# Optimization experiments

Hardware: AMD Instinct MI355X
Metric: run time of the kernel (lower is better)

## Reference

```python
import jax, jax.numpy as jnp
import numpy as np

QLEN, BSZ, HID, NH, HD = 512, 8, 1024, 16, 64
PLEN = 2 * QLEN
SCALE = 1.0 / (HD ** 0.5)
BIG_NUM = 1e30
EPS = 1e-5


def _rel_shift(x, klen):
    # x: [b, n, i, j] -> shifted [b, n, i, klen], same raw-reshape trick as torch.
    b, n, i, j = x.shape
    x = x.reshape(b, n, j, i)[:, :, 1:, :]
    x = x.reshape(b, n, i, j - 1)
    return x[:, :, :, :klen]


def setup_inputs() -> dict:
    key = jax.random.key(0)
    ks = jax.random.split(key, 12)
    s = jnp.float32(0.02)
    return {
        "hidden_states": jax.random.normal(ks[0], (QLEN, BSZ, HID), jnp.float32),
        "position_embed": jax.random.normal(ks[1], (PLEN, BSZ, HID), jnp.float32),
        "segment_embed": jax.random.uniform(ks[2], (QLEN, QLEN, BSZ, 2), jnp.float32),
        "attn_mask": jnp.zeros((QLEN, QLEN, BSZ, 1), jnp.float32),
        "q": jax.random.normal(ks[3], (HID, NH, HD), jnp.float32) * s,
        "k": jax.random.normal(ks[4], (HID, NH, HD), jnp.float32) * s,
        "v": jax.random.normal(ks[5], (HID, NH, HD), jnp.float32) * s,
        "r": jax.random.normal(ks[6], (HID, NH, HD), jnp.float32) * s,
        "o": jax.random.normal(ks[7], (HID, NH, HD), jnp.float32) * s,
        "r_w_bias": jax.random.normal(ks[8], (NH, HD), jnp.float32) * s,
        "r_r_bias": jax.random.normal(ks[9], (NH, HD), jnp.float32) * s,
        "r_s_bias": jax.random.normal(ks[10], (NH, HD), jnp.float32) * s,
        "seg_mat": jax.random.normal(ks[11], (2, NH, HD), jnp.float32) * s,
        "ln_gamma": jnp.ones((HID,), jnp.float32),
        "ln_beta": jnp.zeros((HID,), jnp.float32),
    }


def reference(hidden_states, position_embed, segment_embed, attn_mask,
              q, k, v, r, o, r_w_bias, r_r_bias, r_s_bias, seg_mat,
              ln_gamma, ln_beta):
    query = jnp.einsum('ibh,hnd->ibnd', hidden_states, q)
    key_ = jnp.einsum('ibh,hnd->ibnd', hidden_states, k)
    value = jnp.einsum('ibh,hnd->ibnd', hidden_states, v)
    key_r = jnp.einsum('ibh,hnd->ibnd', position_embed, r)

    # content score
    ac = jnp.einsum('ibnd,jbnd->bnij', query + r_w_bias, key_)
    # relative position score with rel_shift
    bd = jnp.einsum('ibnd,jbnd->bnij', query + r_r_bias, key_r)
    bd = _rel_shift(bd, ac.shape[3])
    # segment score
    ef = jnp.einsum('ibnd,snd->ibns', query + r_s_bias, seg_mat)
    ef = jnp.einsum('ijbs,ibns->bnij', segment_embed, ef)

    attn_score = (ac + bd + ef) * SCALE
    attn_score = attn_score - BIG_NUM * jnp.transpose(attn_mask, (2, 3, 0, 1))
    attn_prob = jax.nn.softmax(attn_score, axis=-1)  # dropout is identity in eval

    attn_out = jnp.einsum('bnij,jbnd->ibnd', attn_prob, value)
    attn_out = jnp.einsum('ibnd,hnd->ibh', attn_out, o)

    x = attn_out + hidden_states
    mu = jnp.mean(x, axis=-1, keepdims=True)
    var = jnp.mean((x - mu) ** 2, axis=-1, keepdims=True)
    return (x - mu) * jax.lax.rsqrt(var + EPS) * ln_gamma + ln_beta
```

## Files before the change

### kernel.cpp

```cpp
#include <hip/hip_runtime.h>
#include <hip/hip_bf16.h>

#define I_LEN 512
#define BSZ   8
#define HIDN  1024
#define NHEAD 16
#define HDIM  64
#define PLEN_ 1024
#define SCALE_F 0.125f
#define BIGNUM 1e30f
#define LN_EPS 1e-5f

typedef unsigned int   u32;
typedef unsigned short u16;
typedef __attribute__((ext_vector_type(8))) short bf16x8;
typedef __attribute__((ext_vector_type(4))) float f32x4;

__device__ __forceinline__ float bflo(u32 w) { return __uint_as_float(w << 16); }
__device__ __forceinline__ float bfhi(u32 w) { return __uint_as_float(w & 0xffff0000u); }
__device__ __forceinline__ u16 f2bf(float x) {
  u32 u = __float_as_uint(x);
  return (u16)((u + 0x7fffu + ((u >> 16) & 1u)) >> 16);
}
__device__ __forceinline__ void bf8_to_f(const uint4 v, float* f) {
  f[0] = bflo(v.x); f[1] = bfhi(v.x);
  f[2] = bflo(v.y); f[3] = bfhi(v.y);
  f[4] = bflo(v.z); f[5] = bfhi(v.z);
  f[6] = bflo(v.w); f[7] = bfhi(v.w);
}

#define GLOAD_LDS16(gp, lp) __builtin_amdgcn_global_load_lds( \
    (const __attribute__((address_space(1))) void*)(gp),      \
    (__attribute__((address_space(3))) void*)(lp), 16, 0, 0)

__global__ __launch_bounds__(256)
void proj_gemm(const u16* __restrict__ Hb, const float* __restrict__ pos,
               const u16* __restrict__ Wqt, const u16* __restrict__ Wkt,
               const u16* __restrict__ Wvt, const u16* __restrict__ Wrt,
               u16* __restrict__ Qh, u16* __restrict__ Kf,
               u16* __restrict__ Vh, u16* __restrict__ Krf) {
  constexpr int K = 1024;
  __shared__ union {
    struct { u16 As[2 * 8192]; u16 Bs[2 * 8192]; } st;
    u16 epi[4][64 * 68];
    u16 epiK[128 * 137];
  } sm;
  u16* As = sm.st.As;
  u16* Bs = sm.st.Bs;
  const int id = blockIdx.x;
  const int low = id & 7;
  const int rest = id >> 3;
  const int bx = rest & 7;
  const int grp = low + 8 * (rest >> 3);
  const int by = grp & 31;
  const int z = grp >> 5;
  const u16* Bt; u16* C;
  if (z == 0)      { Bt = Wqt; C = Qh;  }
  else if (z == 1) { Bt = Wkt; C = Kf;  }
  else if (z == 2) { Bt = Wvt; C = Vh;  }
  else if (z == 3) { Bt = Wrt; C = Krf; }
  else             { Bt = Wrt; C = Krf; }
  const float* Apos = pos + (size_t)((z == 4) ? 4096 : 0) * 1024;
  const int bm = by * 128, bn = bx * 128;
  const int tid = threadIdx.x, wv = tid >> 6, lane = tid & 63;
  const int l15 = lane & 15, g = lane >> 4;
  const int wr = wv >> 1, wc = wv & 1;

#define STAGE_B_P(BUF, K0)                                                    \
  _Pragma("unroll")                                                           \
  for (int p = 0; p < 4; ++p) {                                               \
    const int unit = (wv * 4 + p) * 64 + lane;                                \
    const int row = unit >> 3, up = unit & 7, cc = up ^ (row & 7);            \
    GLOAD_LDS16(&Bt[(size_t)(bn + row) * K + (K0) + cc * 8],                  \
                &Bs[(BUF) * 8192 + unit * 8]);                                \
  }
#define STAGE_A16_P(BUF, K0)                                                  \
  _Pragma("unroll")                                                           \
  for (int p = 0; p < 4; ++p) {                                               \
    const int unit = (wv * 4 + p) * 64 + lane;                                \
    const int row = unit >> 3, up = unit & 7, cc = up ^ (row & 7);            \
    GLOAD_LDS16(&Hb[(size_t)(bm + row) * K + (K0) + cc * 8],                  \
                &As[(BUF) * 8192 + unit * 8]);                                \
  }
#define STAGE_A32_P(BUF, K0)                                                  \
  _Pragma("unroll")                                                           \
  for (int p = 0; p < 4; ++p) {                                               \
    const int unit = p * 256 + tid;                                           \
    const int row = unit >> 3, up = unit & 7, cc = up ^ (row & 7);            \
    const float* src = &Apos[(size_t)(bm + row) * K + (K0) + cc * 8];         \
    const float4 f0 = *(const float4*)src;                                    \
    const float4 f1 = *(const float4*)(src + 4);                              \
    ushort4 h0, h1;                                                           \
    h0.x = f2bf(f0.x); h0.y = f2bf(f0.y); h0.z = f2bf(f0.z); h0.w = f2bf(f0.w); \
    h1.x = f2bf(f1.x); h1.y = f2bf(f1.y); h1.z = f2bf(f1.z); h1.w = f2bf(f1.w); \
    *(ushort4*)&As[(BUF) * 8192 + unit * 8] = h0;                             \
    *(ushort4*)&As[(BUF) * 8192 + unit * 8 + 4] = h1;                         \
  }
#define COMPUTE_TILE(CUR)                                                     \
  {                                                                           \
    const u16* Ac = &As[(CUR) * 8192];                                        \
    const u16* Bc = &Bs[(CUR) * 8192];                                        \
    _Pragma("unroll")                                                         \
    for (int h = 0; h < 2; ++h) {                                             \
      bf16x8 af[4], bfv[4];                                                   \
      _Pragma("unroll")                                                       \
      for (int m = 0; m < 4; ++m) {                                           \
        const int row = wr * 64 + m * 16 + l15;                               \
        af[m] = *(const bf16x8*)&Ac[row * 64 + ((h * 4 + g) ^ (row & 7)) * 8];\
      }                                                                       \
      _Pragma("unroll")                                                       \
      for (int n = 0; n < 4; ++n) {                                           \
        const int col = wc * 64 + n * 16 + l15;                               \
        bfv[n] = *(const bf16x8*)&Bc[col * 64 + ((h * 4 + g) ^ (col & 7)) * 8];\
      }                                                                       \
      _Pragma("unroll")                                                       \
      for (int m = 0; m < 4; ++m)                                             \
        _Pragma("unroll")                                                     \
        for (int n = 0; n < 4; ++n)                                           \
          acc[m][n] = __builtin_amdgcn_mfma_f32_16x16x32_bf16(af[m], bfv[n],  \
                                                              acc[m][n], 0, 0, 0); \
    }                                                                         \
  }

  f32x4 acc[4][4];
#pragma unroll
  for (int m = 0; m < 4; ++m)
#pragma unroll
    for (int n = 0; n < 4; ++n) acc[m][n] = (f32x4){0.f, 0.f, 0.f, 0.f};

  if (z < 3) {
    STAGE_B_P(0, 0);
    STAGE_A16_P(0, 0);
    int cur = 0;
    for (int t = 0; t < 16; ++t) {
      if (t < 15) {
        const int k1 = (t + 1) * 64;
        STAGE_B_P(cur ^ 1, k1);
        STAGE_A16_P(cur ^ 1, k1);
        asm volatile("s_waitcnt vmcnt(8)" ::: "memory");
      } else {
        asm volatile("s_waitcnt vmcnt(0)" ::: "memory");
      }
      __builtin_amdgcn_s_barrier();
      __builtin_amdgcn_sched_barrier(0);
      COMPUTE_TILE(cur);
      __builtin_amdgcn_s_barrier();
      cur ^= 1;
    }
  } else {
    STAGE_B_P(0, 0);
    STAGE_A32_P(0, 0);
    __syncthreads();
    int cur = 0;
    for (int t = 0; t < 16; ++t) {
      if (t < 15) {
        const int k1 = (t + 1) * 64;
        STAGE_B_P(cur ^ 1, k1);
        STAGE_A32_P(cur ^ 1, k1);
      }
      COMPUTE_TILE(cur);
      __syncthreads();
      cur ^= 1;
    }
  }

  if (z == 1 || z >= 3) {
    u16* E128 = sm.epiK;
#pragma unroll
    for (int m = 0; m < 4; ++m)
#pragma unroll
      for (int nf = 0; nf < 4; ++nf)
#pragma unroll
        for (int r = 0; r < 4; ++r)
          E128[(wr * 64 + m * 16 + g * 4 + r) * 137 + wc * 64 + nf * 16 + l15] =
              f2bf(acc[m][nf][r]);
    __syncthreads();
    const int tK = (z == 1) ? by : (by + ((z == 4) ? 32 : 0));
    const int TS = (z == 1) ? 32 : 64;
#pragma unroll
    for (int q = 0; q < 8; ++q) {
      const int rid = wv * 8 + q;
      const int n_loc = rid >> 4, b_ = (rid >> 1) & 7, h = rid & 1;
      union { u16 us[8]; uint4 qv; } o;
#pragma unroll
      for (int e = 0; e < 8; ++e)
        o.us[e] = E128[(l15 * 8 + b_) * 137 + n_loc * 64 + h * 32 + g * 8 + e];
      const int head = bx * 2 + n_loc;
      const size_t base = (((size_t)(b_ * 16 + head) * TS + tK) * 2 + h) * 512 + lane * 8;
      *(uint4*)&C[base] = o.qv;
    }
  } else {
    u16* slice = sm.epi[wv];
    __syncthreads();
#pragma unroll
    for (int m = 0; m < 4; ++m)
#pragma unroll
      for (int nf = 0; nf < 4; ++nf)
#pragma unroll
        for (int r = 0; r < 4; ++r)
          slice[(m * 16 + g * 4 + r) * 68 + nf * 16 + l15] = f2bf(acc[m][nf][r]);
#pragma unroll
    for (int it = 0; it < 8; ++it) {
      const int rl = it * 8 + (lane >> 3);
      const int cl = (lane & 7) * 8;
      const ushort4 a = *(const ushort4*)&slice[rl * 68 + cl];
      const ushort4 b2 = *(const ushort4*)&slice[rl * 68 + cl + 4];
      const int row = bm + wr * 64 + rl;
      const int col = bn + wc * 64 + cl;
      const size_t idx = ((size_t)((row & 7) * 16 + (col >> 6)) * 512 + (row >> 3)) * 64 + (col & 63);
      *(ushort4*)&C[idx] = a;
      *(ushort4*)&C[idx + 4] = b2;
    }
  }
}

__global__ __launch_bounds__(256)
void vrepack_kernel(u16* __restrict__ V) {
  __shared__ u16 tile[64][72];
  const int bn = blockIdx.x, slab = blockIdx.y;
  const int t = threadIdx.x;
  const size_t base = ((size_t)bn * 8 + slab) * 4096;
  {
    const int jl = t >> 2, c0 = (t & 3) * 16;
    const uint4 v0 = *(const uint4*)&V[base + jl * 64 + c0];
    const uint4 v1 = *(const uint4*)&V[base + jl * 64 + c0 + 8];
    *(uint4*)&tile[jl][c0] = v0;
    *(uint4*)&tile[jl][c0 + 8] = v1;
  }
  __syncthreads();
  const int lane = t & 63, g = lane >> 4, l15 = lane & 15;
#pragma unroll
  for (int w = 0; w < 2; ++w) {
    const int run = w * 4 + (t >> 6);
    const int c = run >> 1, h = run & 1;
    union { u16 us[8]; uint4 qv; } o;
#pragma unroll
    for (int e = 0; e < 8; ++e) o.us[e] = tile[h * 32 + g * 8 + e][16 * c + l15];
    *(uint4*)&V[base + run * 512 + lane * 8] = o.qv;
  }
}

__global__ __launch_bounds__(256)
void hcvt_kernel(const float* __restrict__ hidden, const float* __restrict__ ow,
                 u16* __restrict__ Hb, u16* __restrict__ Wob) {
  const size_t i = (size_t)blockIdx.x * 256 + threadIdx.x;
  const float* src; u16* dst; size_t off;
  if (i < 524288) { src = hidden; dst = Hb; off = i * 8; }
  else            { src = ow;     dst = Wob; off = (i - 524288) * 8; }
  const float4 a = *(const float4*)&src[off];
  const float4 b = *(const float4*)&src[off + 4];
  ushort4 o0, o1;
  o0.x = f2bf(a.x); o0.y = f2bf(a.y); o0.z = f2bf(a.z); o0.w = f2bf(a.w);
  o1.x = f2bf(b.x); o1.y = f2bf(b.y); o1.z = f2bf(b.z); o1.w = f2bf(b.w);
  *(ushort4*)&dst[off] = o0;
  *(ushort4*)&dst[off + 4] = o1;
}

__global__ __launch_bounds__(256)
void wtrans_kernel(const float* __restrict__ W0, const float* __restrict__ W1,
                   const float* __restrict__ W2, const float* __restrict__ W3,
                   u16* __restrict__ T0, u16* __restrict__ T1,
                   u16* __restrict__ T2, u16* __restrict__ T3) {
  __shared__ u16 tile[64][72];
  const int z = blockIdx.z;
  const float* W = (z == 0) ? W0 : ((z == 1) ? W1 : ((z == 2) ? W2 : W3));
  u16* T = (z == 0) ? T0 : ((z == 1) ? T1 : ((z == 2) ? T2 : T3));
  const int h0 = blockIdx.y * 64, nd0 = blockIdx.x * 64;
  const int t = threadIdx.x;
  {
    const int hr = t >> 2, c0 = (t & 3) * 16;
#pragma unroll
    for (int q = 0; q < 4; ++q) {
      const float4 f = *(const float4*)&W[(size_t)(h0 + hr) * 1024 + nd0 + c0 + q * 4];
      tile[hr][c0 + q * 4 + 0] = f2bf(f.x);
      tile[hr][c0 + q * 4 + 1] = f2bf(f.y);
      tile[hr][c0 + q * 4 + 2] = f2bf(f.z);
      tile[hr][c0 + q * 4 + 3] = f2bf(f.w);
    }
  }
  __syncthreads();
  const int ndr = t >> 2, hc0 = (t & 3) * 16;
  union { u16 us[16]; uint4 qv[2]; } o;
#pragma unroll
  for (int e = 0; e < 16; ++e) o.us[e] = tile[hc0 + e][ndr];
  uint4* dst = (uint4*)&T[(size_t)(nd0 + ndr) * 1024 + h0 + hc0];
  dst[0] = o.qv[0]; dst[1] = o.qv[1];
}

__global__ __launch_bounds__(256)
void setrans_kernel(const float* __restrict__ sege, const float* __restrict__ amask,
                    u16* __restrict__ SE4, u16* __restrict__ MK) {
  const int i = blockIdx.x;
  const int j = blockIdx.y * 256 + threadIdx.x;
  const float* sp = &sege[((size_t)i * 512 + j) * 16];
  const float* mp = &amask[((size_t)i * 512 + j) * 8];
  float se[16], mk[8];
#pragma unroll
  for (int q = 0; q < 4; ++q) {
    const float4 f = *(const float4*)(sp + q * 4);
    se[q * 4 + 0] = f.x; se[q * 4 + 1] = f.y; se[q * 4 + 2] = f.z; se[q * 4 + 3] = f.w;
  }
#pragma unroll
  for (int q = 0; q < 2; ++q) {
    const float4 f = *(const float4*)(mp + q * 4);
    mk[q * 4 + 0] = f.x; mk[q * 4 + 1] = f.y; mk[q * 4 + 2] = f.z; mk[q * 4 + 3] = f.w;
  }
#pragma unroll
  for (int b = 0; b < 8; ++b) {
    const u32 pk = (u32)f2bf(se[b * 2]) | ((u32)f2bf(se[b * 2 + 1]) << 16);
    const size_t plane = ((size_t)b * 512 + i) * 512 + j;
    *(u32*)&SE4[plane * 2] = pk;
    MK[plane] = f2bf(BIGNUM * mk[b]);
  }
}

__global__ __launch_bounds__(256)
void seg_e_kernel(const u16* __restrict__ Qh, const float* __restrict__ rsb,
                  const float* __restrict__ segm, float* __restrict__ E) {
  const int gt = blockIdx.x * 256 + threadIdx.x;
  const int i = gt >> 7, bb = (gt >> 4) & 7, n = gt & 15;
  const size_t base = (((size_t)bb * 16 + n) * 512 + i) * 64;
  float e0 = 0.f, e1 = 0.f;
#pragma unroll
  for (int u8 = 0; u8 < 8; ++u8) {
    const uint4 qv = *(const uint4*)&Qh[base + u8 * 8];
    float qf[8];
    bf8_to_f(qv, qf);
#pragma unroll
    for (int w = 0; w < 8; ++w) {
      const int d = u8 * 8 + w;
      const float q = qf[w] + rsb[n * HDIM + d];
      e0 += q * segm[n * HDIM + d];
      e1 += q * segm[HIDN + n * HDIM + d];
    }
  }
  E[(size_t)gt * 2 + 0] = e0;
  E[(size_t)gt * 2 + 1] = e1;
}

__global__ __launch_bounds__(256)
void attn_mfma(const u16* __restrict__ Qh, const u16* __restrict__ Kf,
               const u16* __restrict__ Vf, const u16* __restrict__ Krf,
               const float* __restrict__ E, const u16* __restrict__ SE4,
               const u16* __restrict__ MK, const float* __restrict__ rwb,
               const float* __restrict__ rrb, u16* __restrict__ AOb) {
  __shared__ u16 Pl[4][16 * 64];
  const int id = blockIdx.x;
  const int b = id & 7, n = (id >> 3) & 15;
  const int i0 = (id >> 7) * 64;
  const int bn = b * 16 + n;
  const int t = threadIdx.x, wv = t >> 6, lane = t & 63;
  const int l15 = lane & 15, g = lane >> 4;
  const int irow0 = i0 + wv * 16;
  u16* Pw = Pl[wv];
  const int bn64 = bn * 64;

  bf16x8 qcf[2], qrf[2];
#pragma unroll
  for (int h = 0; h < 2; ++h) {
    const int d0 = 32 * h + g * 8;
    const uint4 qv = *(const uint4*)&Qh[((size_t)bn * 512 + irow0 + l15) * 64 + d0];
    float qf[8]; bf8_to_f(qv, qf);
    union { u16 us[8]; bf16x8 v; } ua, ub;
#pragma unroll
    for (int w = 0; w < 8; ++w) {
      ua.us[w] = f2bf((qf[w] + rwb[n * HDIM + d0 + w]) * SCALE_F);
      ub.us[w] = f2bf((qf[w] + rrb[n * HDIM + d0 + w]) * SCALE_F);
    }
    qcf[h] = ua.v; qrf[h] = ub.v;
  }

  float e0v[4], e1v[4], lrun[4];
  f32x4 accO[4];
#pragma unroll
  for (int r = 0; r < 4; ++r) {
    const int i = irow0 + 4 * g + r;
    const float2 ee = *(const float2*)&E[((size_t)(i * BSZ + b) * NHEAD + n) * 2];
    e0v[r] = ee.x * SCALE_F; e1v[r] = ee.y * SCALE_F;
    lrun[r] = 0.f;
  }
#pragma unroll
  for (int c = 0; c < 4; ++c) accO[c] = (f32x4){0.f, 0.f, 0.f, 0.f};

  for (int jb = 0; jb < I_LEN; jb += 64) {
    u32 sev[4][4]; u16 mkv[4][4];
#pragma unroll
    for (int c = 0; c < 4; ++c)
#pragma unroll
      for (int r = 0; r < 4; ++r) {
        const size_t plane = ((size_t)b * 512 + (irow0 + 4 * g + r)) * 512 + jb + 16 * c + l15;
        sev[c][r] = *(const u32*)&SE4[plane * 2];
        mkv[c][r] = MK[plane];
      }
    bf16x8 vf[4][2];
#pragma unroll
    for (int c = 0; c < 4; ++c) {
      const u16* vp = &Vf[((((size_t)bn * 8 + (jb >> 6)) * 4 + c) * 2) * 512 + lane * 8];
      vf[c][0] = *(const bf16x8*)vp;
      vf[c][1] = *(const bf16x8*)(vp + 512);
    }
    f32x4 S[4];
#pragma unroll
    for (int c = 0; c < 4; ++c) S[c] = (f32x4){0.f, 0.f, 0.f, 0.f};
#pragma unroll
    for (int c = 0; c < 4; ++c) {
      const u16* kp = &Kf[(((size_t)bn * 32 + (jb >> 4) + c) * 2) * 512 + lane * 8];
      S[c] = __builtin_amdgcn_mfma_f32_16x16x32_bf16(qcf[0], *(const bf16x8*)kp, S[c], 0, 0, 0);
      S[c] = __builtin_amdgcn_mfma_f32_16x16x32_bf16(qcf[1], *(const bf16x8*)(kp + 512), S[c], 0, 0, 0);
    }
    const int tb = (jb + 496 - irow0) >> 4;
    f32x4 T[5];
#pragma unroll
    for (int c = 0; c < 5; ++c) T[c] = (f32x4){0.f, 0.f, 0.f, 0.f};
#pragma unroll
    for (int c = 0; c < 5; ++c) {
      const u16* kp = &Krf[(((size_t)bn * 64 + tb + c) * 2) * 512 + lane * 8];
      T[c] = __builtin_amdgcn_mfma_f32_16x16x32_bf16(qrf[0], *(const bf16x8*)kp, T[c], 0, 0, 0);
      T[c] = __builtin_amdgcn_mfma_f32_16x16x32_bf16(qrf[1], *(const bf16x8*)(kp + 512), T[c], 0, 0, 0);
    }
    float bd[4][4];
#pragma unroll
    for (int r = 0; r < 4; ++r) {
      const int ii = 4 * g + r;
      const int pos = (lane & 48) | ((l15 - ii) & 15);
      float bp[5];
#pragma unroll
      for (int c = 0; c < 5; ++c) bp[c] = __shfl(T[c][r], pos, 64);
      const bool sel = l15 >= ii;
#pragma unroll
      for (int c = 0; c < 4; ++c) bd[c][r] = sel ? bp[c + 1] : bp[c];
    }
#pragma unroll
    for (int c = 0; c < 4; ++c)
#pragma unroll
      for (int r = 0; r < 4; ++r) {
        const u32 sev_ = sev[c][r];
        const float s = S[c][r] + bd[c][r] + bflo(sev_) * e0v[r] + bfhi(sev_) * e1v[r]
                        - bflo((u32)mkv[c][r]);
        const float p = __expf(s);
        S[c][r] = p;
        lrun[r] += p;
      }
#pragma unroll
    for (int c = 0; c < 4; ++c)
#pragma unroll
      for (int r = 0; r < 4; ++r) {
        const int ii = 4 * g + r;
        Pw[ii * 64 + ((16 * c + l15) ^ ((ii & 7) << 3))] = f2bf(S[c][r]);
      }
    const bf16x8 pa0 = *(const bf16x8*)&Pw[l15 * 64 + ((g * 8) ^ ((l15 & 7) << 3))];
    const bf16x8 pa1 = *(const bf16x8*)&Pw[l15 * 64 + ((32 + g * 8) ^ ((l15 & 7) << 3))];
#pragma unroll
    for (int c = 0; c < 4; ++c) {
      accO[c] = __builtin_amdgcn_mfma_f32_16x16x32_bf16(pa0, vf[c][0], accO[c], 0, 0, 0);
      accO[c] = __builtin_amdgcn_mfma_f32_16x16x32_bf16(pa1, vf[c][1], accO[c], 0, 0, 0);
    }
  }
#pragma unroll
  for (int r = 0; r < 4; ++r) {
#pragma unroll
    for (int o = 1; o < 16; o <<= 1) lrun[r] += __shfl_xor(lrun[r], o);
  }
#pragma unroll
  for (int c = 0; c < 4; ++c)
#pragma unroll
    for (int r = 0; r < 4; ++r) {
      const int ii = 4 * g + r;
      AOb[(size_t)(irow0 + ii) * 8192 + bn64 + 16 * c + l15] = f2bf(accO[c][r] / lrun[r]);
    }
}

__global__ __launch_bounds__(256)
void oproj_gemm(const u16* __restrict__ A, const u16* __restrict__ Wob,
                const float* __restrict__ Res, float* __restrict__ C) {
  constexpr int K = 1024;
  __shared__ u16 As[2 * 4096];
  __shared__ u16 Bs[2 * 8192];
  const int id = blockIdx.x;
  const int low = id & 7;
  const int rest = id >> 3;
  const int bx = rest & 7;
  const int by = low + 8 * (rest >> 3);
  const int bm = by * 64, bn = bx * 128;
  const int tid = threadIdx.x, wv = tid >> 6, lane = tid & 63;
  const int l15 = lane & 15, g = lane >> 4;
  const int wr = wv >> 1, wc = wv & 1;

#define STAGE_O(BUF, K0)                                                      \
  _Pragma("unroll")                                                           \
  for (int p = 0; p < 2; ++p) {                                               \
    const int unit = (wv * 2 + p) * 64 + lane;                                \
    const int row = unit >> 3, up = unit & 7, cc = up ^ (row & 7);            \
    GLOAD_LDS16(&A[(size_t)(bm + row) * K + (K0) + cc * 8],                   \
                &As[(BUF) * 4096 + unit * 8]);                                \
  }                                                                           \
  _Pragma("unroll")                                                           \
  for (int p = 0; p < 4; ++p) {                                               \
    const int unit = (wv * 4 + p) * 64 + lane;                                \
    const int row = unit >> 3, up = unit & 7, cc = up ^ (row & 7);            \
    GLOAD_LDS16(&Wob[(size_t)(bn + row) * K + (K0) + cc * 8],                 \
                &Bs[(BUF) * 8192 + unit * 8]);                                \
  }

  f32x4 acc[2][4];
#pragma unroll
  for (int m = 0; m < 2; ++m)
#pragma unroll
    for (int n = 0; n < 4; ++n) acc[m][n] = (f32x4){0.f, 0.f, 0.f, 0.f};

  STAGE_O(0, 0);
  int cur = 0;
  for (int t = 0; t < 16; ++t) {
    if (t < 15) {
      STAGE_O(cur ^ 1, (t + 1) * 64);
      asm volatile("s_waitcnt vmcnt(6)" ::: "memory");
    } else {
      asm volatile("s_waitcnt vmcnt(0)" ::: "memory");
    }
    __builtin_amdgcn_s_barrier();
    __builtin_amdgcn_sched_barrier(0);
    const u16* Ac = &As[cur * 4096];
    const u16* Bc = &Bs[cur * 8192];
#pragma unroll
    for (int h = 0; h < 2; ++h) {
      bf16x8 af[2], bfv[4];
#pragma unroll
      for (int m = 0; m < 2; ++m) {
        const int row = wr * 32 + m * 16 + l15;
        af[m] = *(const bf16x8*)&Ac[row * 64 + ((h * 4 + g) ^ (row & 7)) * 8];
      }
#pragma unroll
      for (int n = 0; n < 4; ++n) {
        const int col = wc * 64 + n * 16 + l15;
        bfv[n] = *(const bf16x8*)&Bc[col * 64 + ((h * 4 + g) ^ (col & 7)) * 8];
      }
#pragma unroll
      for (int m = 0; m < 2; ++m)
#pragma unroll
        for (int n = 0; n < 4; ++n)
          acc[m][n] = __builtin_amdgcn_mfma_f32_16x16x32_bf16(af[m], bfv[n], acc[m][n], 0, 0, 0);
    }
    __builtin_amdgcn_s_barrier();
    cur ^= 1;
  }
#pragma unroll
  for (int m = 0; m < 2; ++m) {
    const int row0 = bm + wr * 32 + m * 16 + g * 4;
#pragma unroll
    for (int nf = 0; nf < 4; ++nf) {
      const int col = bn + wc * 64 + nf * 16 + l15;
#pragma unroll
      for (int r = 0; r < 4; ++r) {
        const int row = row0 + r;
        C[(size_t)row * 1024 + col] = acc[m][nf][r] + Res[(size_t)row * 1024 + col];
      }
    }
  }
}

__global__ __launch_bounds__(256)
void ln_kernel(const float* __restrict__ X, const float* __restrict__ gam,
               const float* __restrict__ bet, float* __restrict__ out) {
  const int row = blockIdx.x, t = threadIdx.x;
  const float4 x4 = *(const float4*)&X[(size_t)row * HIDN + t * 4];
  float s  = x4.x + x4.y + x4.z + x4.w;
  float sq = x4.x * x4.x + x4.y * x4.y + x4.z * x4.z + x4.w * x4.w;
#pragma unroll
  for (int o = 32; o >= 1; o >>= 1) { s += __shfl_xor(s, o); sq += __shfl_xor(sq, o); }
  __shared__ float red[8];
  const int wv = t >> 6;
  if ((t & 63) == 0) { red[wv * 2] = s; red[wv * 2 + 1] = sq; }
  __syncthreads();
  s  = red[0] + red[2] + red[4] + red[6];
  sq = red[1] + red[3] + red[5] + red[7];
  const float mu  = s * (1.f / HIDN);
  const float var = sq * (1.f / HIDN) - mu * mu;
  const float rs  = rsqrtf(var + LN_EPS);
  const float4 g4 = *(const float4*)&gam[t * 4];
  const float4 b4 = *(const float4*)&bet[t * 4];
  float4 o4;
  o4.x = (x4.x - mu) * rs * g4.x + b4.x;
  o4.y = (x4.y - mu) * rs * g4.y + b4.y;
  o4.z = (x4.z - mu) * rs * g4.z + b4.z;
  o4.w = (x4.w - mu) * rs * g4.w + b4.w;
  *(float4*)&out[(size_t)row * HIDN + t * 4] = o4;
}

extern "C" void kernel_launch(void* const* d_in, const int* in_sizes, int n_in,
                              void* d_out, int out_size, void* d_ws, size_t ws_size,
                              hipStream_t stream) {
  (void)in_sizes; (void)n_in; (void)out_size; (void)ws_size;
  const float* hidden = (const float*)d_in[0];
  const float* pos    = (const float*)d_in[1];
  const float* sege   = (const float*)d_in[2];
  const float* amask  = (const float*)d_in[3];
  const float* qw     = (const float*)d_in[4];
  const float* kw     = (const float*)d_in[5];
  const float* vw     = (const float*)d_in[6];
  const float* rw     = (const float*)d_in[7];
  const float* ow     = (const float*)d_in[8];
  const float* rwb    = (const float*)d_in[9];
  const float* rrb    = (const float*)d_in[10];
  const float* rsb    = (const float*)d_in[11];
  const float* segm   = (const float*)d_in[12];
  const float* gam    = (const float*)d_in[13];
  const float* bet    = (const float*)d_in[14];
  float* out = (float*)d_out;
  char* ws = (char*)d_ws;

  const size_t MiB = 1ull << 20;
  u16*   Wqt = (u16*)(ws);
  u16*   Wkt = (u16*)(ws + 2 * MiB);
  u16*   Wvt = (u16*)(ws + 4 * MiB);
  u16*   Wrt = (u16*)(ws + 6 * MiB);
  u16*   AOb = (u16*)(ws);
  u16*   Qh  = (u16*)(ws + 8 * MiB);
  u16*   Kf  = (u16*)(ws + 16 * MiB);
  u16*   Vf  = (u16*)(ws + 24 * MiB);
  u16*   Krf = (u16*)(ws + 32 * MiB);
  float* X   = (float*)(ws + 32 * MiB);
  u16*   Hb  = (u16*)(ws + 48 * MiB);
  u16*   SE4 = (u16*)(ws + 48 * MiB);
  u16*   MK  = (u16*)(ws + 56 * MiB);
  float* E   = (float*)(ws + 60 * MiB);
  u16*   Wob = (u16*)(ws + 60 * MiB + 512 * 1024);

  wtrans_kernel<<<dim3(16, 16, 4), 256, 0, stream>>>(qw, kw, vw, rw, Wqt, Wkt, Wvt, Wrt);
  hcvt_kernel<<<2560, 256, 0, stream>>>(hidden, ow, Hb, Wob);
  proj_gemm<<<1280, 256, 0, stream>>>(Hb, pos, Wqt, Wkt, Wvt, Wrt, Qh, Kf, Vf, Krf);
  vrepack_kernel<<<dim3(128, 8), 256, 0, stream>>>(Vf);
  setrans_kernel<<<dim3(512, 2), 256, 0, stream>>>(sege, amask, SE4, MK);
  seg_e_kernel<<<256, 256, 0, stream>>>(Qh, rsb, segm, E);
  attn_mfma<<<1024, 256, 0, stream>>>(Qh, Kf, Vf, Krf, E, SE4, MK, rwb, rrb, AOb);
  oproj_gemm<<<512, 256, 0, stream>>>(AOb, Wob, hidden, X);
  ln_kernel<<<4096, 256, 0, stream>>>(X, gam, bet, out);
}
```

Measured before the change: 159.7 us.

## Merge prep kernels and fold segment transpose into projection GEMM grid

Weight transpose and the hidden/o-weight bf16 conversion are combined into one prep_kernel launch, and V repack plus the segment E computation share a single post_kernel. When the workspace is large enough, the segment/mask transpose runs as extra blocks of the projection GEMM, writing to a separate buffer so it no longer aliases Hb. In attention, the QK and QKr MFMAs are moved ahead of the segment, mask and V loads to overlap those loads with compute. This cuts launch count and tail gaps, in exchange for more branching per kernel and higher register or workspace pressure.

```diff
diff --git a/kernel.cpp b/kernel.cpp
--- a/kernel.cpp
+++ b/kernel.cpp
@@ -33,12 +33,99 @@
     (const __attribute__((address_space(1))) void*)(gp),      \
     (__attribute__((address_space(3))) void*)(lp), 16, 0, 0)
 
+__device__ __forceinline__ void setrans_body(int i, int j,
+    const float* __restrict__ sege, const float* __restrict__ amask,
+    u16* __restrict__ SE4, u16* __restrict__ MK) {
+  const float* sp = &sege[((size_t)i * 512 + j) * 16];
+  const float* mp = &amask[((size_t)i * 512 + j) * 8];
+  float se[16], mk[8];
+#pragma unroll
+  for (int q = 0; q < 4; ++q) {
+    const float4 f = *(const float4*)(sp + q * 4);
+    se[q * 4 + 0] = f.x; se[q * 4 + 1] = f.y; se[q * 4 + 2] = f.z; se[q * 4 + 3] = f.w;
+  }
+#pragma unroll
+  for (int q = 0; q < 2; ++q) {
+    const float4 f = *(const float4*)(mp + q * 4);
+    mk[q * 4 + 0] = f.x; mk[q * 4 + 1] = f.y; mk[q * 4 + 2] = f.z; mk[q * 4 + 3] = f.w;
+  }
+#pragma unroll
+  for (int b = 0; b < 8; ++b) {
+    const u32 pk = (u32)f2bf(se[b * 2]) | ((u32)f2bf(se[b * 2 + 1]) << 16);
+    const size_t plane = ((size_t)b * 512 + i) * 512 + j;
+    *(u32*)&SE4[plane * 2] = pk;
+    MK[plane] = f2bf(BIGNUM * mk[b]);
+  }
+}
+
+__global__ __launch_bounds__(256)
+void setrans_kernel(const float* __restrict__ sege, const float* __restrict__ amask,
+                    u16* __restrict__ SE4, u16* __restrict__ MK) {
+  const int blk = blockIdx.x;
+  setrans_body(blk & 511, (blk >> 9) * 256 + threadIdx.x, sege, amask, SE4, MK);
+}
+
+__global__ __launch_bounds__(256)
+void prep_kernel(const float* __restrict__ W0, const float* __restrict__ W1,
+                 const float* __restrict__ W2, const float* __restrict__ W3,
+                 u16* __restrict__ T0, u16* __restrict__ T1,
+                 u16* __restrict__ T2, u16* __restrict__ T3,
+                 const float* __restrict__ hidden, const float* __restrict__ ow,
+                 u16* __restrict__ Hb, u16* __restrict__ Wob) {
+  const int blk = blockIdx.x;
+  const int t = threadIdx.x;
+  if (blk >= 1024) {
+    const size_t i = (size_t)(blk - 1024) * 256 + t;
+    const float* src; u16* dst; size_t off;
+    if (i < 524288) { src = hidden; dst = Hb;  off = i * 8; }
+    else            { src = ow;     dst = Wob; off = (i - 524288) * 8; }
+    const float4 a = *(const float4*)&src[off];
+    const float4 b = *(const float4*)&src[off + 4];
+    ushort4 o0, o1;
+    o0.x = f2bf(a.x); o0.y = f2bf(a.y); o0.z = f2bf(a.z); o0.w = f2bf(a.w);
+    o1.x = f2bf(b.x); o1.y = f2bf(b.y); o1.z = f2bf(b.z); o1.w = f2bf(b.w);
+    *(ushort4*)&dst[off] = o0;
+    *(ushort4*)&dst[off + 4] = o1;
+    return;
+  }
+  __shared__ u16 tile[64][72];
+  const int x = blk & 15, y = (blk >> 4) & 15, z = blk >> 8;
+  const float* W = (z == 0) ? W0 : ((z == 1) ? W1 : ((z == 2) ? W2 : W3));
+  u16* T = (z == 0) ? T0 : ((z == 1) ? T1 : ((z == 2) ? T2 : T3));
+  const int h0 = y * 64, nd0 = x * 64;
+  {
+    const int hr = t >> 2, c0 = (t & 3) * 16;
+#pragma unroll
+    for (int q = 0; q < 4; ++q) {
+      const float4 f = *(const float4*)&W[(size_t)(h0 + hr) * 1024 + nd0 + c0 + q * 4];
+      tile[hr][c0 + q * 4 + 0] = f2bf(f.x);
+      tile[hr][c0 + q * 4 + 1] = f2bf(f.y);
+      tile[hr][c0 + q * 4 + 2] = f2bf(f.z);
+      tile[hr][c0 + q * 4 + 3] = f2bf(f.w);
+    }
+  }
+  __syncthreads();
+  const int ndr = t >> 2, hc0 = (t & 3) * 16;
+  union { u16 us[16]; uint4 qv[2]; } o;
+#pragma unroll
+  for (int e = 0; e < 16; ++e) o.us[e] = tile[hc0 + e][ndr];
+  uint4* dst = (uint4*)&T[(size_t)(nd0 + ndr) * 1024 + h0 + hc0];
+  dst[0] = o.qv[0]; dst[1] = o.qv[1];
+}
+
 __global__ __launch_bounds__(256)
 void proj_gemm(const u16* __restrict__ Hb, const float* __restrict__ pos,
                const u16* __restrict__ Wqt, const u16* __restrict__ Wkt,
                const u16* __restrict__ Wvt, const u16* __restrict__ Wrt,
                u16* __restrict__ Qh, u16* __restrict__ Kf,
-               u16* __restrict__ Vh, u16* __restrict__ Krf) {
+               u16* __restrict__ Vh, u16* __restrict__ Krf,
+               const float* __restrict__ sege, const float* __restrict__ amask,
+               u16* __restrict__ SE4, u16* __restrict__ MK) {
+  if (blockIdx.x >= 1280) {
+    const int sid = blockIdx.x - 1280;
+    setrans_body(sid & 511, (sid >> 9) * 256 + threadIdx.x, sege, amask, SE4, MK);
+    return;
+  }
   constexpr int K = 1024;
   __shared__ union {
     struct { u16 As[2 * 8192]; u16 Bs[2 * 8192]; } st;
@@ -215,10 +302,35 @@
 }
 
 __global__ __launch_bounds__(256)
-void vrepack_kernel(u16* __restrict__ V) {
+void post_kernel(u16* __restrict__ V, const u16* __restrict__ Qh,
+                 const float* __restrict__ rsb, const float* __restrict__ segm,
+                 float* __restrict__ E) {
+  const int blk = blockIdx.x;
+  const int t = threadIdx.x;
+  if (blk >= 1024) {
+    const int gt = (blk - 1024) * 256 + t;
+    const int i = gt >> 7, bb = (gt >> 4) & 7, n = gt & 15;
+    const size_t base = (((size_t)bb * 16 + n) * 512 + i) * 64;
+    float e0 = 0.f, e1 = 0.f;
+#pragma unroll
+    for (int u8 = 0; u8 < 8; ++u8) {
+      const uint4 qv = *(const uint4*)&Qh[base + u8 * 8];
+      float qf[8];
+      bf8_to_f(qv, qf);
+#pragma unroll
+      for (int w = 0; w < 8; ++w) {
+        const int d = u8 * 8 + w;
+        const float q = qf[w] + rsb[n * HDIM + d];
+        e0 += q * segm[n * HDIM + d];
+        e1 += q * segm[HIDN + n * HDIM + d];
+      }
+    }
+    E[(size_t)gt * 2 + 0] = e0;
+    E[(size_t)gt * 2 + 1] = e1;
+    return;
+  }
   __shared__ u16 tile[64][72];
-  const int bn = blockIdx.x, slab = blockIdx.y;
-  const int t = threadIdx.x;
+  const int bn = blk & 127, slab = blk >> 7;
   const size_t base = ((size_t)bn * 8 + slab) * 4096;
   {
     const int jl = t >> 2, c0 = (t & 3) * 16;
@@ -238,104 +350,6 @@
     for (int e = 0; e < 8; ++e) o.us[e] = tile[h * 32 + g * 8 + e][16 * c + l15];
     *(uint4*)&V[base + run * 512 + lane * 8] = o.qv;
   }
-}
-
-__global__ __launch_bounds__(256)
-void hcvt_kernel(const float* __restrict__ hidden, const float* __restrict__ ow,
-                 u16* __restrict__ Hb, u16* __restrict__ Wob) {
-  const size_t i = (size_t)blockIdx.x * 256 + threadIdx.x;
-  const float* src; u16* dst; size_t off;
-  if (i < 524288) { src = hidden; dst = Hb; off = i * 8; }
-  else            { src = ow;     dst = Wob; off = (i - 524288) * 8; }
-  const float4 a = *(const float4*)&src[off];
-  const float4 b = *(const float4*)&src[off + 4];
-  ushort4 o0, o1;
-  o0.x = f2bf(a.x); o0.y = f2bf(a.y); o0.z = f2bf(a.z); o0.w = f2bf(a.w);
-  o1.x = f2bf(b.x); o1.y = f2bf(b.y); o1.z = f2bf(b.z); o1.w = f2bf(b.w);
-  *(ushort4*)&dst[off] = o0;
-  *(ushort4*)&dst[off + 4] = o1;
-}
-
-__global__ __launch_bounds__(256)
-void wtrans_kernel(const float* __restrict__ W0, const float* __restrict__ W1,
-                   const float* __restrict__ W2, const float* __restrict__ W3,
-                   u16* __restrict__ T0, u16* __restrict__ T1,
-                   u16* __restrict__ T2, u16* __restrict__ T3) {
-  __shared__ u16 tile[64][72];
-  const int z = blockIdx.z;
-  const float* W = (z == 0) ? W0 : ((z == 1) ? W1 : ((z == 2) ? W2 : W3));
-  u16* T = (z == 0) ? T0 : ((z == 1) ? T1 : ((z == 2) ? T2 : T3));
-  const int h0 = blockIdx.y * 64, nd0 = blockIdx.x * 64;
-  const int t = threadIdx.x;
-  {
-    const int hr = t >> 2, c0 = (t & 3) * 16;
-#pragma unroll
-    for (int q = 0; q < 4; ++q) {
-      const float4 f = *(const float4*)&W[(size_t)(h0 + hr) * 1024 + nd0 + c0 + q * 4];
-      tile[hr][c0 + q * 4 + 0] = f2bf(f.x);
-      tile[hr][c0 + q * 4 + 1] = f2bf(f.y);
-      tile[hr][c0 + q * 4 + 2] = f2bf(f.z);
-      tile[hr][c0 + q * 4 + 3] = f2bf(f.w);
-    }
-  }
-  __syncthreads();
-  const int ndr = t >> 2, hc0 = (t & 3) * 16;
-  union { u16 us[16]; uint4 qv[2]; } o;
-#pragma unroll
-  for (int e = 0; e < 16; ++e) o.us[e] = tile[hc0 + e][ndr];
-  uint4* dst = (uint4*)&T[(size_t)(nd0 + ndr) * 1024 + h0 + hc0];
-  dst[0] = o.qv[0]; dst[1] = o.qv[1];
-}
-
-__global__ __launch_bounds__(256)
-void setrans_kernel(const float* __restrict__ sege, const float* __restrict__ amask,
-                    u16* __restrict__ SE4, u16* __restrict__ MK) {
-  const int i = blockIdx.x;
-  const int j = blockIdx.y * 256 + threadIdx.x;
-  const float* sp = &sege[((size_t)i * 512 + j) * 16];
-  const float* mp = &amask[((size_t)i * 512 + j) * 8];
-  float se[16], mk[8];
-#pragma unroll
-  for (int q = 0; q < 4; ++q) {
-    const float4 f = *(const float4*)(sp + q * 4);
-    se[q * 4 + 0] = f.x; se[q * 4 + 1] = f.y; se[q * 4 + 2] = f.z; se[q * 4 + 3] = f.w;
-  }
-#pragma unroll
-  for (int q = 0; q < 2; ++q) {
-    const float4 f = *(const float4*)(mp + q * 4);
-    mk[q * 4 + 0] = f.x; mk[q * 4 + 1] = f.y; mk[q * 4 + 2] = f.z; mk[q * 4 + 3] = f.w;
-  }
-#pragma unroll
-  for (int b = 0; b < 8; ++b) {
-    const u32 pk = (u32)f2bf(se[b * 2]) | ((u32)f2bf(se[b * 2 + 1]) << 16);
-    const size_t plane = ((size_t)b * 512 + i) * 512 + j;
-    *(u32*)&SE4[plane * 2] = pk;
-    MK[plane] = f2bf(BIGNUM * mk[b]);
-  }
-}
-
-__global__ __launch_bounds__(256)
-void seg_e_kernel(const u16* __restrict__ Qh, const float* __restrict__ rsb,
-                  const float* __restrict__ segm, float* __restrict__ E) {
-  const int gt = blockIdx.x * 256 + threadIdx.x;
-  const int i = gt >> 7, bb = (gt >> 4) & 7, n = gt & 15;
-  const size_t base = (((size_t)bb * 16 + n) * 512 + i) * 64;
-  float e0 = 0.f, e1 = 0.f;
-#pragma unroll
-  for (int u8 = 0; u8 < 8; ++u8) {
-    const uint4 qv = *(const uint4*)&Qh[base + u8 * 8];
-    float qf[8];
-    bf8_to_f(qv, qf);
-#pragma unroll
-    for (int w = 0; w < 8; ++w) {
-      const int d = u8 * 8 + w;
-      const float q = qf[w] + rsb[n * HDIM + d];
-      e0 += q * segm[n * HDIM + d];
-      e1 += q * segm[HIDN + n * HDIM + d];
-    }
-  }
-  E[(size_t)gt * 2 + 0] = e0;
-  E[(size_t)gt * 2 + 1] = e1;
 }
 
 __global__ __launch_bounds__(256)
@@ -383,6 +397,25 @@
   for (int c = 0; c < 4; ++c) accO[c] = (f32x4){0.f, 0.f, 0.f, 0.f};
 
   for (int jb = 0; jb < I_LEN; jb += 64) {
+    f32x4 S[4];
+#pragma unroll
+    for (int c = 0; c < 4; ++c) S[c] = (f32x4){0.f, 0.f, 0.f, 0.f};
+#pragma unroll
+    for (int c = 0; c < 4; ++c) {
+      const u16* kp = &Kf[(((size_t)bn * 32 + (jb >> 4) + c) * 2) * 512 + lane * 8];
+      S[c] = __builtin_amdgcn_mfma_f32_16x16x32_bf16(qcf[0], *(const bf16x8*)kp, S[c], 0, 0, 0);
+      S[c] = __builtin_amdgcn_mfma_f32_16x16x32_bf16(qcf[1], *(const bf16x8*)(kp + 512), S[c], 0, 0, 0);
+    }
+    const int tb = (jb + 496 - irow0) >> 4;
+    f32x4 T[5];
+#pragma unroll
+    for (int c = 0; c < 5; ++c) T[c] = (f32x4){0.f, 0.f, 0.f, 0.f};
+#pragma unroll
+    for (int c = 0; c < 5; ++c) {
+      const u16* kp = &Krf[(((size_t)bn * 64 + tb + c) * 2) * 512 + lane * 8];
+      T[c] = __builtin_amdgcn_mfma_f32_16x16x32_bf16(qrf[0], *(const bf16x8*)kp, T[c], 0, 0, 0);
+      T[c] = __builtin_amdgcn_mfma_f32_16x16x32_bf16(qrf[1], *(const bf16x8*)(kp + 512), T[c], 0, 0, 0);
+    }
     u32 sev[4][4]; u16 mkv[4][4];
 #pragma unroll
     for (int c = 0; c < 4; ++c)
@@ -398,25 +431,6 @@
       const u16* vp = &Vf[((((size_t)bn * 8 + (jb >> 6)) * 4 + c) * 2) * 512 + lane * 8];
       vf[c][0] = *(const bf16x8*)vp;
       vf[c][1] = *(const bf16x8*)(vp + 512);
-    }
-    f32x4 S[4];
-#pragma unroll
-    for (int c = 0; c < 4; ++c) S[c] = (f32x4){0.f, 0.f, 0.f, 0.f};
-#pragma unroll
-    for (int c = 0; c < 4; ++c) {
-      const u16* kp = &Kf[(((size_t)bn * 32 + (jb >> 4) + c) * 2) * 512 + lane * 8];
-      S[c] = __builtin_amdgcn_mfma_f32_16x16x32_bf16(qcf[0], *(const bf16x8*)kp, S[c], 0, 0, 0);
-      S[c] = __builtin_amdgcn_mfma_f32_16x16x32_bf16(qcf[1], *(const bf16x8*)(kp + 512), S[c], 0, 0, 0);
-    }
-    const int tb = (jb + 496 - irow0) >> 4;
-    f32x4 T[5];
-#pragma unroll
-    for (int c = 0; c < 5; ++c) T[c] = (f32x4){0.f, 0.f, 0.f, 0.f};
-#pragma unroll
-    for (int c = 0; c < 5; ++c) {
-      const u16* kp = &Krf[(((size_t)bn * 64 + tb + c) * 2) * 512 + lane * 8];
-      T[c] = __builtin_amdgcn_mfma_f32_16x16x32_bf16(qrf[0], *(const bf16x8*)kp, T[c], 0, 0, 0);
-      T[c] = __builtin_amdgcn_mfma_f32_16x16x32_bf16(qrf[1], *(const bf16x8*)(kp + 512), T[c], 0, 0, 0);
     }
     float bd[4][4];
 #pragma unroll
@@ -589,7 +603,7 @@
 extern "C" void kernel_launch(void* const* d_in, const int* in_sizes, int n_in,
                               void* d_out, int out_size, void* d_ws, size_t ws_size,
                               hipStream_t stream) {
-  (void)in_sizes; (void)n_in; (void)out_size; (void)ws_size;
+  (void)in_sizes; (void)n_in; (void)out_size;
   const float* hidden = (const float*)d_in[0];
   const float* pos    = (const float*)d_in[1];
   const float* sege   = (const float*)d_in[2];
@@ -620,17 +634,22 @@
   u16*   Krf = (u16*)(ws + 32 * MiB);
   float* X   = (float*)(ws + 32 * MiB);
   u16*   Hb  = (u16*)(ws + 48 * MiB);
-  u16*   SE4 = (u16*)(ws + 48 * MiB);
+  u16*   SE4_lo = (u16*)(ws + 48 * MiB);
   u16*   MK  = (u16*)(ws + 56 * MiB);
   float* E   = (float*)(ws + 60 * MiB);
   u16*   Wob = (u16*)(ws + 60 * MiB + 512 * 1024);
-
-  wtrans_kernel<<<dim3(16, 16, 4), 256, 0, stream>>>(qw, kw, vw, rw, Wqt, Wkt, Wvt, Wrt);
-  hcvt_kernel<<<2560, 256, 0, stream>>>(hidden, ow, Hb, Wob);
-  proj_gemm<<<1280, 256, 0, stream>>>(Hb, pos, Wqt, Wkt, Wvt, Wrt, Qh, Kf, Vf, Krf);
-  vrepack_kernel<<<dim3(128, 8), 256, 0, stream>>>(Vf);
-  setrans_kernel<<<dim3(512, 2), 256, 0, stream>>>(sege, amask, SE4, MK);
-  seg_e_kernel<<<256, 256, 0, stream>>>(Qh, rsb, segm, E);
+  u16*   SE4_hi = (u16*)(ws + 62 * MiB + 512 * 1024);
+
+  const bool merged = ws_size >= (70 * MiB + 512 * 1024 + 4096);
+  u16* SE4 = merged ? SE4_hi : SE4_lo;
+
+  prep_kernel<<<3584, 256, 0, stream>>>(qw, kw, vw, rw, Wqt, Wkt, Wvt, Wrt,
+                                        hidden, ow, Hb, Wob);
+  proj_gemm<<<merged ? 2304 : 1280, 256, 0, stream>>>(
+      Hb, pos, Wqt, Wkt, Wvt, Wrt, Qh, Kf, Vf, Krf, sege, amask, SE4, MK);
+  if (!merged)
+    setrans_kernel<<<1024, 256, 0, stream>>>(sege, amask, SE4, MK);
+  post_kernel<<<1280, 256, 0, stream>>>(Vf, Qh, rsb, segm, E);
   attn_mfma<<<1024, 256, 0, stream>>>(Qh, Kf, Vf, Krf, E, SE4, MK, rwb, rrb, AOb);
   oproj_gemm<<<512, 256, 0, stream>>>(AOb, Wob, hidden, X);
   ln_kernel<<<4096, 256, 0, stream>>>(X, gam, bet, out);
```

After: 164.5 us. +3.0%, slower.
